# Kernel tuning notes

Measured on AMD Instinct MI355X. Metric: run time of the kernel, lower is better.

Reference implementation:

```python
import jax, jax.numpy as jnp
import numpy as np

N_IMG = 1024
N_VIEWS = 90


def _bilinear(img, yi, xi):
    """Bilinear sample img at float coords (yi=row, xi=col); 0 outside (skimage warp cval=0)."""
    n = img.shape[0]
    y0 = jnp.floor(yi)
    x0 = jnp.floor(xi)
    wy = yi - y0
    wx = xi - x0
    y0i = y0.astype(jnp.int32)
    x0i = x0.astype(jnp.int32)

    def get(yy, xx):
        valid = (yy >= 0) & (yy < n) & (xx >= 0) & (xx < n)
        v = img[jnp.clip(yy, 0, n - 1), jnp.clip(xx, 0, n - 1)]
        return jnp.where(valid, v, jnp.zeros((), img.dtype))

    v00 = get(y0i, x0i)
    v01 = get(y0i, x0i + 1)
    v10 = get(y0i + 1, x0i)
    v11 = get(y0i + 1, x0i + 1)
    return (v00 * (1 - wy) * (1 - wx) + v01 * (1 - wy) * wx
            + v10 * wy * (1 - wx) + v11 * wy * wx)


def radon_jax(image, theta_deg):
    """skimage.transform.radon(image, theta, circle=True) equivalent.
    Rotate image by each angle (bilinear, about center = N//2, inverse map as in
    skimage warp) and sum over rows. Returns sinogram [N, n_angles]."""
    n = image.shape[0]
    center = n // 2
    ang = jnp.deg2rad(theta_deg.astype(image.dtype))
    cos_a = jnp.cos(ang)  # [A]
    sin_a = jnp.sin(ang)
    coords = jnp.arange(n, dtype=image.dtype)
    X, Y = jnp.meshgrid(coords, coords)  # X = col (x), Y = row (y), [N, N]

    def rotate_and_sum(ca, sa):
        # inverse map: src = R @ dst (homogeneous, (x, y) order) as in skimage radon
        x_in = ca * X + sa * Y - center * (ca + sa - 1)
        y_in = -sa * X + ca * Y - center * (ca - sa - 1)
        rotated = _bilinear(image, y_in, x_in)  # [N, N]
        return rotated.sum(axis=0)  # sum over rows -> projection [N]

    sino = jax.vmap(rotate_and_sum)(cos_a, sin_a)  # [A, N]
    return sino.T  # [N, A] to match skimage radon layout


def setup_inputs() -> dict:
    key = jax.random.key(0)
    k1, _ = jax.random.split(key)
    x = jax.random.normal(k1, (N_IMG, N_IMG), dtype=jnp.float32)
    theta = jnp.arange(N_VIEWS, dtype=jnp.float32) * 2.0  # 0..178 deg, 2-deg spacing
    return {"x": x, "theta": theta}


def reference(x, theta):
    return radon_jax(x, theta)
```

## Files before the change

kernel.cpp:

```cpp
#include <hip/hip_runtime.h>

#define N_IMG   1024
#define N_VIEWS 90
#define CENTER  512
#define TILE    64
#define NYB     (N_IMG / TILE)
#define NTHREADS 512
#define NWAVES   8
#define YPT      (TILE / NWAVES)
#define TILE_WORDS 9216

typedef float v2f __attribute__((ext_vector_type(2)));

__device__ __forceinline__ void map_coords(float ca, float sa, float cx, float cy,
                                           float Xf, float Yf,
                                           float& x_in, float& y_in) {
    const float fx0 = fmaf(ca, Xf, cx);
    const float fy0 = fmaf(-sa, Xf, cy);
    x_in = fmaf(sa, Yf, fx0);
    y_in = fmaf(ca, Yf, fy0);
}

__device__ __forceinline__ void gload_lds4(const float* g, float* l) {
    __builtin_amdgcn_global_load_lds((const __attribute__((address_space(1))) void*)g,
                                     (__attribute__((address_space(3))) void*)l, 4, 0, 0);
}
__device__ __forceinline__ void gload_lds16(const float* g, float* l) {
    __builtin_amdgcn_global_load_lds((const __attribute__((address_space(1))) void*)g,
                                     (__attribute__((address_space(3))) void*)l, 16, 0, 0);
}

template<int STRIDE>
__device__ __forceinline__ float sample_tile(const float* __restrict__ tile,
                                             float sa, float ca,
                                             float x_in, float y_in, float basef) {
    const float Sf = (float)STRIDE;
    v2f x2 = {x_in, x_in + sa};
    v2f y2 = {y_in, y_in + ca};
    const v2f dx2 = {2.0f * sa, 2.0f * sa};
    const v2f dy2 = {2.0f * ca, 2.0f * ca};
    const v2f S2  = {Sf, Sf};
    const v2f b2  = {basef, basef};
    v2f acc2 = {0.0f, 0.0f};
    #pragma unroll
    for (int p = 0; p < YPT / 2; ++p) {
        v2f x0f = {floorf(x2.x), floorf(x2.y)};
        v2f y0f = {floorf(y2.x), floorf(y2.y)};
        const v2f wx = x2 - x0f;
        const v2f wy = y2 - y0f;
        const v2f lif = y0f * S2 + x0f + b2;
        const int li0 = (int)lif.x;
        const int li1 = (int)lif.y;
        const v2f t00 = {tile[li0],              tile[li1]};
        const v2f t01 = {tile[li0 + 1],          tile[li1 + 1]};
        const v2f t10 = {tile[li0 + STRIDE],     tile[li1 + STRIDE]};
        const v2f t11 = {tile[li0 + STRIDE + 1], tile[li1 + STRIDE + 1]};
        const v2f top = (t01 - t00) * wx + t00;
        const v2f bot = (t11 - t10) * wx + t10;
        acc2 += (bot - top) * wy + top;
        x2 += dx2; y2 += dy2;
    }
    return acc2.x + acc2.y;
}

__global__ __launch_bounds__(NTHREADS) void radon_tile(const float* __restrict__ img,
                                                       const float* __restrict__ theta,
                                                       float* __restrict__ partial,
                                                       float* __restrict__ out,
                                                       int mode) {
    __shared__ float tile[TILE_WORDS];
    __shared__ float fpar[4];
    __shared__ int   ipar[8];

    const int a  = blockIdx.z;
    const int X0 = blockIdx.x * TILE;
    const int Y0 = blockIdx.y * TILE;
    const int tid  = threadIdx.x;
    const int lane = tid & 63;
    const int wv   = tid >> 6;

    if (wv == 0) {
        const float ang = theta[a] * 0.017453292519943295f;
        float sa, ca;
        __sincosf(ang, &sa, &ca);
        const float cx = (float)CENTER * (1.0f - ca - sa);
        const float cy = (float)CENTER * (1.0f - ca + sa);

        float x00, y00, x01, y01, x10, y10, x11, y11;
        map_coords(ca, sa, cx, cy, (float)X0,        (float)Y0,        x00, y00);
        map_coords(ca, sa, cx, cy, (float)(X0 + 63), (float)Y0,        x01, y01);
        map_coords(ca, sa, cx, cy, (float)X0,        (float)(Y0 + 63), x10, y10);
        map_coords(ca, sa, cx, cy, (float)(X0 + 63), (float)(Y0 + 63), x11, y11);
        const float xmin = fminf(fminf(x00, x01), fminf(x10, x11));
        const float xmax = fmaxf(fmaxf(x00, x01), fmaxf(x10, x11));
        const float ymin = fminf(fminf(y00, y01), fminf(y10, y11));
        const float ymax = fmaxf(fmaxf(y00, y01), fmaxf(y10, y11));

        const int ix0_raw = (int)floorf(xmin);
        const int ix1_raw = (int)floorf(xmax) + 1;
        const int iy0_raw = (int)floorf(ymin);
        const int iy1_raw = (int)floorf(ymax) + 1;

        const bool empty = (ix1_raw < 0) || (ix0_raw > N_IMG - 1) ||
                           (iy1_raw < 0) || (iy0_raw > N_IMG - 1);
        const bool interior = (ix0_raw >= 0) && (ix1_raw <= N_IMG - 1) &&
                              (iy0_raw >= 0) && (iy1_raw <= N_IMG - 1);

        int path = (fabsf(ca) > 0.7072f) ? 0 : ((ca > 0.0f) ? 1 : 2);
        int iy0w, win, dB = 0, ry0 = 0, nrows = 0;
        if (interior) {
            iy0w = iy0_raw;
            if (path == 0) {
                win = min(ix0_raw & ~3, N_IMG - 96);
            } else {
                win = min(ix0_raw, N_IMG - 64);
                dB  = max(win, ix1_raw - 63) - win;
            }
            nrows = iy1_raw - iy0_raw + 1;
        } else {
            iy0w = iy0_raw;
            win  = ix0_raw & ~3;
            ry0  = max(0, iy0_raw);
            nrows = min(N_IMG - 1, iy1_raw) - ry0 + 1;
        }
        if (tid == 0) {
            fpar[0] = sa; fpar[1] = ca; fpar[2] = cx; fpar[3] = cy;
            ipar[0] = iy0w; ipar[1] = nrows; ipar[2] = win; ipar[3] = dB;
            ipar[4] = path;
            ipar[5] = empty ? 1 : (interior ? 2 : 0);
            ipar[6] = ry0;
        }
    }
    __syncthreads();

    float* __restrict__ pslot = partial + ((size_t)(a * NYB + blockIdx.y) << 10) + X0;
    const int flags = ipar[5];

    if (flags & 1) {
        if (mode == 0 && tid < 64) pslot[tid] = 0.0f;
        return;
    }

    const float sa = fpar[0], ca = fpar[1], cx = fpar[2], cy = fpar[3];
    const int iy0 = ipar[0], nrows = ipar[1], win = ipar[2], dB = ipar[3];
    const int path = ipar[4];
    const int S = (path == 0) ? 96 : ((path == 1) ? 95 : 97);

    if (flags & 2) {
        if (path == 0) {
            const int D = nrows * 96;
            for (int o = wv * 256; o < D; o += NWAVES * 256) {
                const int d = o + 4 * lane;
                const int r = (unsigned)d / 96u;
                const int c = d - r * 96;
                const int gr = min(iy0 + r, N_IMG - 1);
                gload_lds16(img + (size_t)gr * N_IMG + win + c, tile + o);
            }
        } else {
            const float* g = img + (size_t)(iy0 + wv) * N_IMG + win + lane;
            float* l = tile + wv * S;
            for (int r = wv; r < nrows; r += NWAVES) {
                gload_lds4(g, l);
                if (dB > 0) gload_lds4(g + dB, l + dB);
                g += NWAVES * N_IMG;
                l += NWAVES * S;
            }
        }
    } else {
        for (int o4 = tid; o4 < TILE_WORDS / 4; o4 += NTHREADS)
            *(float4*)(tile + 4 * o4) = make_float4(0.f, 0.f, 0.f, 0.f);
        __syncthreads();
        const int ry0 = ipar[6];
        const int cx0 = max(0, win);
        const int cxe = min(N_IMG - 1, win + 94);
        const int wIn = cxe - cx0 + 1;
        const int n4  = wIn >> 2;
        const int items = nrows * 24;
        for (int idx = tid; idx < items; idx += NTHREADS) {
            const int r  = (unsigned)idx / 24u;
            const int c4 = idx - r * 24;
            const int gy = ry0 + r;
            float* dst = tile + (gy - iy0) * S + (cx0 - win) + 4 * c4;
            const float* src = img + (size_t)gy * N_IMG + cx0 + 4 * c4;
            if (c4 < n4) {
                *(float4*)dst = *(const float4*)src;
            } else if (c4 == n4) {
                for (int j = 0; j < (wIn & 3); ++j) dst[j] = src[j];
            }
        }
    }
    __syncthreads();

    const float Xf  = (float)(X0 + lane);
    const float fx0 = fmaf(ca, Xf, cx);
    const float fy0 = fmaf(-sa, Xf, cy);
    const float Ybf = (float)(Y0 + wv * YPT);
    const float x_in = fmaf(sa, Ybf, fx0);
    const float y_in = fmaf(ca, Ybf, fy0);
    const float basef = -(float)(iy0 * S + win);

    float acc;
    if (path == 0)      acc = sample_tile<96>(tile, sa, ca, x_in, y_in, basef);
    else if (path == 1) acc = sample_tile<95>(tile, sa, ca, x_in, y_in, basef);
    else                acc = sample_tile<97>(tile, sa, ca, x_in, y_in, basef);

    __syncthreads();
    tile[wv * 64 + lane] = acc;
    __syncthreads();
    if (wv == 0) {
        float s = 0.0f;
        #pragma unroll
        for (int w = 0; w < NWAVES; ++w) s += tile[w * 64 + lane];
        if (mode == 0) pslot[lane] = s;
        else           atomicAdd(&out[(X0 + lane) * N_VIEWS + a], s);
    }
}

__global__ __launch_bounds__(256) void reduce_partials(const float* __restrict__ partial,
                                                       float* __restrict__ out) {
    const int g = blockIdx.x * 256 + threadIdx.x;
    const int a = g >> 10;
    const int X = g & 1023;
    float s = 0.0f;
    #pragma unroll
    for (int yb = 0; yb < NYB; ++yb)
        s += partial[((size_t)(a * NYB + yb) << 10) + X];
    out[X * N_VIEWS + a] = s;
}

extern "C" void kernel_launch(void* const* d_in, const int* in_sizes, int n_in,
                              void* d_out, int out_size, void* d_ws, size_t ws_size,
                              hipStream_t stream) {
    const float* img   = (const float*)d_in[0];
    const float* theta = (const float*)d_in[1];
    float* out     = (float*)d_out;
    float* partial = (float*)d_ws;

    const size_t needed = (size_t)N_VIEWS * NYB * N_IMG * sizeof(float);
    const int mode = (ws_size >= needed) ? 0 : 1;
    if (mode == 1)
        (void)hipMemsetAsync(d_out, 0, (size_t)out_size * sizeof(float), stream);

    dim3 grid(N_IMG / TILE, N_IMG / TILE, N_VIEWS);
    radon_tile<<<grid, NTHREADS, 0, stream>>>(img, theta, partial, out, mode);

    if (mode == 0)
        reduce_partials<<<(N_VIEWS * N_IMG) / 256, 256, 0, stream>>>(partial, out);
}
```

Before: 140.4 us.

## Fuse Y-tile loop into one block per column strip with double-buffered LDS

Each block now handles one angle and one 64-column strip, looping over all 16 Y tiles. While one LDS buffer is sampled, the next tile's image window is prefetched into the other. Per-tile bounds are computed in parallel across lanes and broadcast with shuffles. This removes the partial-sum workspace, the separate reduction kernel and its launch. The cost is a grid of only 1440 blocks, double the LDS per block (which limits occupancy), and serialized per-tile work inside each block.

```diff
diff --git a/kernel.cpp b/kernel.cpp
--- a/kernel.cpp
+++ b/kernel.cpp
@@ -4,7 +4,7 @@
 #define N_VIEWS 90
 #define CENTER  512
 #define TILE    64
-#define NYB     (N_IMG / TILE)
+#define NTX     (N_IMG / TILE)
 #define NTHREADS 512
 #define NWAVES   8
 #define YPT      (TILE / NWAVES)
@@ -63,169 +63,161 @@
     return acc2.x + acc2.y;
 }
 
-__global__ __launch_bounds__(NTHREADS) void radon_tile(const float* __restrict__ img,
-                                                       const float* __restrict__ theta,
-                                                       float* __restrict__ partial,
-                                                       float* __restrict__ out,
-                                                       int mode) {
-    __shared__ float tile[TILE_WORDS];
-    __shared__ float fpar[4];
-    __shared__ int   ipar[8];
-
-    const int a  = blockIdx.z;
-    const int X0 = blockIdx.x * TILE;
-    const int Y0 = blockIdx.y * TILE;
+struct JobP { int win, dB, iy0, nrows, ry0, fl; };
+
+__global__ __launch_bounds__(NTHREADS, 4) void radon_fused(const float* __restrict__ img,
+                                                           const float* __restrict__ theta,
+                                                           float* __restrict__ out) {
+    __shared__ float tile[2][TILE_WORDS];
+
+    const int bx  = blockIdx.x;
+    const int a   = bx >> 4;
+    const int tx  = bx & (NTX - 1);
+    const int X0  = tx * TILE;
     const int tid  = threadIdx.x;
     const int lane = tid & 63;
     const int wv   = tid >> 6;
 
-    if (wv == 0) {
-        const float ang = theta[a] * 0.017453292519943295f;
-        float sa, ca;
-        __sincosf(ang, &sa, &ca);
-        const float cx = (float)CENTER * (1.0f - ca - sa);
-        const float cy = (float)CENTER * (1.0f - ca + sa);
-
-        float x00, y00, x01, y01, x10, y10, x11, y11;
-        map_coords(ca, sa, cx, cy, (float)X0,        (float)Y0,        x00, y00);
-        map_coords(ca, sa, cx, cy, (float)(X0 + 63), (float)Y0,        x01, y01);
-        map_coords(ca, sa, cx, cy, (float)X0,        (float)(Y0 + 63), x10, y10);
-        map_coords(ca, sa, cx, cy, (float)(X0 + 63), (float)(Y0 + 63), x11, y11);
-        const float xmin = fminf(fminf(x00, x01), fminf(x10, x11));
-        const float xmax = fmaxf(fmaxf(x00, x01), fmaxf(x10, x11));
-        const float ymin = fminf(fminf(y00, y01), fminf(y10, y11));
-        const float ymax = fmaxf(fmaxf(y00, y01), fmaxf(y10, y11));
-
-        const int ix0_raw = (int)floorf(xmin);
-        const int ix1_raw = (int)floorf(xmax) + 1;
-        const int iy0_raw = (int)floorf(ymin);
-        const int iy1_raw = (int)floorf(ymax) + 1;
-
-        const bool empty = (ix1_raw < 0) || (ix0_raw > N_IMG - 1) ||
-                           (iy1_raw < 0) || (iy0_raw > N_IMG - 1);
-        const bool interior = (ix0_raw >= 0) && (ix1_raw <= N_IMG - 1) &&
-                              (iy0_raw >= 0) && (iy1_raw <= N_IMG - 1);
-
-        int path = (fabsf(ca) > 0.7072f) ? 0 : ((ca > 0.0f) ? 1 : 2);
-        int iy0w, win, dB = 0, ry0 = 0, nrows = 0;
-        if (interior) {
-            iy0w = iy0_raw;
+    const float ang = theta[a] * 0.017453292519943295f;
+    float sa, ca;
+    __sincosf(ang, &sa, &ca);
+    const float cx = (float)CENTER * (1.0f - ca - sa);
+    const float cy = (float)CENTER * (1.0f - ca + sa);
+    const int path = (fabsf(ca) > 0.7072f) ? 0 : ((ca > 0.0f) ? 1 : 2);
+    const int S = (path == 0) ? 96 : ((path == 1) ? 95 : 97);
+
+    const int tyl = lane & 15;
+    const float Ybase = (float)(tyl * TILE);
+    float x00, y00, x01, y01, x10, y10, x11, y11;
+    map_coords(ca, sa, cx, cy, (float)X0,        Ybase,        x00, y00);
+    map_coords(ca, sa, cx, cy, (float)(X0 + 63), Ybase,        x01, y01);
+    map_coords(ca, sa, cx, cy, (float)X0,        Ybase + 63.f, x10, y10);
+    map_coords(ca, sa, cx, cy, (float)(X0 + 63), Ybase + 63.f, x11, y11);
+    const float xmin = fminf(fminf(x00, x01), fminf(x10, x11));
+    const float xmax = fmaxf(fmaxf(x00, x01), fmaxf(x10, x11));
+    const float ymin = fminf(fminf(y00, y01), fminf(y10, y11));
+    const float ymax = fmaxf(fmaxf(y00, y01), fmaxf(y10, y11));
+
+    const int ix0_raw = (int)floorf(xmin);
+    const int ix1_raw = (int)floorf(xmax) + 1;
+    const int iy0_raw = (int)floorf(ymin);
+    const int iy1_raw = (int)floorf(ymax) + 1;
+
+    const bool empty = (ix1_raw < 0) || (ix0_raw > N_IMG - 1) ||
+                       (iy1_raw < 0) || (iy0_raw > N_IMG - 1);
+    const bool interior = (ix0_raw >= 0) && (ix1_raw <= N_IMG - 1) &&
+                          (iy0_raw >= 0) && (iy1_raw <= N_IMG - 1);
+
+    int winl, dBl = 0, ry0l = 0, nrl = 0, iy0l = iy0_raw;
+    if (interior) {
+        if (path == 0) {
+            winl = min(ix0_raw & ~3, N_IMG - 96);
+        } else {
+            winl = min(ix0_raw, N_IMG - 64);
+            dBl  = max(winl, ix1_raw - 63) - winl;
+        }
+        nrl = iy1_raw - iy0_raw + 1;
+    } else {
+        winl = ix0_raw & ~3;
+        ry0l = max(0, iy0_raw);
+        nrl  = min(N_IMG - 1, iy1_raw) - ry0l + 1;
+    }
+    const int fll = empty ? 1 : (interior ? 2 : 0);
+
+    auto fetch = [&](int ty) -> JobP {
+        JobP p;
+        p.win   = __shfl(winl, ty);
+        p.dB    = __shfl(dBl,  ty);
+        p.iy0   = __shfl(iy0l, ty);
+        p.nrows = __shfl(nrl,  ty);
+        p.ry0   = __shfl(ry0l, ty);
+        p.fl    = __shfl(fll,  ty);
+        return p;
+    };
+
+    auto stage = [&](const JobP& p, float* buf) {
+        if (p.fl & 1) return;
+        if (p.fl & 2) {
             if (path == 0) {
-                win = min(ix0_raw & ~3, N_IMG - 96);
+                const int D = p.nrows * 96;
+                for (int o = wv * 256; o < D; o += NWAVES * 256) {
+                    const int d = o + 4 * lane;
+                    const int r = (unsigned)d / 96u;
+                    const int c = d - r * 96;
+                    const int gr = min(p.iy0 + r, N_IMG - 1);
+                    gload_lds16(img + (size_t)gr * N_IMG + p.win + c, buf + o);
+                }
             } else {
-                win = min(ix0_raw, N_IMG - 64);
-                dB  = max(win, ix1_raw - 63) - win;
-            }
-            nrows = iy1_raw - iy0_raw + 1;
-        } else {
-            iy0w = iy0_raw;
-            win  = ix0_raw & ~3;
-            ry0  = max(0, iy0_raw);
-            nrows = min(N_IMG - 1, iy1_raw) - ry0 + 1;
-        }
-        if (tid == 0) {
-            fpar[0] = sa; fpar[1] = ca; fpar[2] = cx; fpar[3] = cy;
-            ipar[0] = iy0w; ipar[1] = nrows; ipar[2] = win; ipar[3] = dB;
-            ipar[4] = path;
-            ipar[5] = empty ? 1 : (interior ? 2 : 0);
-            ipar[6] = ry0;
-        }
-    }
-    __syncthreads();
-
-    float* __restrict__ pslot = partial + ((size_t)(a * NYB + blockIdx.y) << 10) + X0;
-    const int flags = ipar[5];
-
-    if (flags & 1) {
-        if (mode == 0 && tid < 64) pslot[tid] = 0.0f;
-        return;
-    }
-
-    const float sa = fpar[0], ca = fpar[1], cx = fpar[2], cy = fpar[3];
-    const int iy0 = ipar[0], nrows = ipar[1], win = ipar[2], dB = ipar[3];
-    const int path = ipar[4];
-    const int S = (path == 0) ? 96 : ((path == 1) ? 95 : 97);
-
-    if (flags & 2) {
-        if (path == 0) {
-            const int D = nrows * 96;
-            for (int o = wv * 256; o < D; o += NWAVES * 256) {
-                const int d = o + 4 * lane;
-                const int r = (unsigned)d / 96u;
-                const int c = d - r * 96;
-                const int gr = min(iy0 + r, N_IMG - 1);
-                gload_lds16(img + (size_t)gr * N_IMG + win + c, tile + o);
+                const float* g = img + (size_t)(p.iy0 + wv) * N_IMG + p.win + lane;
+                float* l = buf + wv * S;
+                for (int r = wv; r < p.nrows; r += NWAVES) {
+                    gload_lds4(g, l);
+                    if (p.dB > 0) gload_lds4(g + p.dB, l + p.dB);
+                    g += NWAVES * N_IMG;
+                    l += NWAVES * S;
+                }
             }
         } else {
-            const float* g = img + (size_t)(iy0 + wv) * N_IMG + win + lane;
-            float* l = tile + wv * S;
-            for (int r = wv; r < nrows; r += NWAVES) {
-                gload_lds4(g, l);
-                if (dB > 0) gload_lds4(g + dB, l + dB);
-                g += NWAVES * N_IMG;
-                l += NWAVES * S;
+            for (int o4 = tid; o4 < TILE_WORDS / 4; o4 += NTHREADS)
+                *(float4*)(buf + 4 * o4) = make_float4(0.f, 0.f, 0.f, 0.f);
+            __syncthreads();
+            const int cx0 = max(0, p.win);
+            const int cxe = min(N_IMG - 1, p.win + 94);
+            const int wIn = cxe - cx0 + 1;
+            const int n4  = wIn >> 2;
+            const int items = p.nrows * 24;
+            for (int idx = tid; idx < items; idx += NTHREADS) {
+                const int r  = (unsigned)idx / 24u;
+                const int c4 = idx - r * 24;
+                const int gy = p.ry0 + r;
+                float* dst = buf + (gy - p.iy0) * S + (cx0 - p.win) + 4 * c4;
+                const float* src = img + (size_t)gy * N_IMG + cx0 + 4 * c4;
+                if (c4 < n4) {
+                    *(float4*)dst = *(const float4*)src;
+                } else if (c4 == n4) {
+                    for (int j = 0; j < (wIn & 3); ++j) dst[j] = src[j];
+                }
             }
         }
-    } else {
-        for (int o4 = tid; o4 < TILE_WORDS / 4; o4 += NTHREADS)
-            *(float4*)(tile + 4 * o4) = make_float4(0.f, 0.f, 0.f, 0.f);
-        __syncthreads();
-        const int ry0 = ipar[6];
-        const int cx0 = max(0, win);
-        const int cxe = min(N_IMG - 1, win + 94);
-        const int wIn = cxe - cx0 + 1;
-        const int n4  = wIn >> 2;
-        const int items = nrows * 24;
-        for (int idx = tid; idx < items; idx += NTHREADS) {
-            const int r  = (unsigned)idx / 24u;
-            const int c4 = idx - r * 24;
-            const int gy = ry0 + r;
-            float* dst = tile + (gy - iy0) * S + (cx0 - win) + 4 * c4;
-            const float* src = img + (size_t)gy * N_IMG + cx0 + 4 * c4;
-            if (c4 < n4) {
-                *(float4*)dst = *(const float4*)src;
-            } else if (c4 == n4) {
-                for (int j = 0; j < (wIn & 3); ++j) dst[j] = src[j];
-            }
-        }
-    }
-    __syncthreads();
+    };
 
     const float Xf  = (float)(X0 + lane);
     const float fx0 = fmaf(ca, Xf, cx);
     const float fy0 = fmaf(-sa, Xf, cy);
-    const float Ybf = (float)(Y0 + wv * YPT);
-    const float x_in = fmaf(sa, Ybf, fx0);
-    const float y_in = fmaf(ca, Ybf, fy0);
-    const float basef = -(float)(iy0 * S + win);
-
-    float acc;
-    if (path == 0)      acc = sample_tile<96>(tile, sa, ca, x_in, y_in, basef);
-    else if (path == 1) acc = sample_tile<95>(tile, sa, ca, x_in, y_in, basef);
-    else                acc = sample_tile<97>(tile, sa, ca, x_in, y_in, basef);
-
+    float acc = 0.0f;
+
+    JobP pc = fetch(0);
+    stage(pc, tile[0]);
     __syncthreads();
-    tile[wv * 64 + lane] = acc;
+
+    for (int ty = 0; ty < 16; ++ty) {
+        JobP pn = pc;
+        if (ty < 15) {
+            pn = fetch(ty + 1);
+            stage(pn, tile[(ty + 1) & 1]);
+        }
+        if (!(pc.fl & 1)) {
+            const float Ybf  = (float)(ty * TILE + wv * YPT);
+            const float x_in = fmaf(sa, Ybf, fx0);
+            const float y_in = fmaf(ca, Ybf, fy0);
+            const float basef = -(float)(pc.iy0 * S + pc.win);
+            const float* tl = tile[ty & 1];
+            if (path == 0)      acc += sample_tile<96>(tl, sa, ca, x_in, y_in, basef);
+            else if (path == 1) acc += sample_tile<95>(tl, sa, ca, x_in, y_in, basef);
+            else                acc += sample_tile<97>(tl, sa, ca, x_in, y_in, basef);
+        }
+        __syncthreads();
+        pc = pn;
+    }
+
+    tile[0][wv * 64 + lane] = acc;
     __syncthreads();
     if (wv == 0) {
         float s = 0.0f;
         #pragma unroll
-        for (int w = 0; w < NWAVES; ++w) s += tile[w * 64 + lane];
-        if (mode == 0) pslot[lane] = s;
-        else           atomicAdd(&out[(X0 + lane) * N_VIEWS + a], s);
-    }
-}
-
-__global__ __launch_bounds__(256) void reduce_partials(const float* __restrict__ partial,
-                                                       float* __restrict__ out) {
-    const int g = blockIdx.x * 256 + threadIdx.x;
-    const int a = g >> 10;
-    const int X = g & 1023;
-    float s = 0.0f;
-    #pragma unroll
-    for (int yb = 0; yb < NYB; ++yb)
-        s += partial[((size_t)(a * NYB + yb) << 10) + X];
-    out[X * N_VIEWS + a] = s;
+        for (int w = 0; w < NWAVES; ++w) s += tile[0][w * 64 + lane];
+        out[(X0 + lane) * N_VIEWS + a] = s;
+    }
 }
 
 extern "C" void kernel_launch(void* const* d_in, const int* in_sizes, int n_in,
@@ -233,17 +225,8 @@
                               hipStream_t stream) {
     const float* img   = (const float*)d_in[0];
     const float* theta = (const float*)d_in[1];
-    float* out     = (float*)d_out;
-    float* partial = (float*)d_ws;
-
-    const size_t needed = (size_t)N_VIEWS * NYB * N_IMG * sizeof(float);
-    const int mode = (ws_size >= needed) ? 0 : 1;
-    if (mode == 1)
-        (void)hipMemsetAsync(d_out, 0, (size_t)out_size * sizeof(float), stream);
-
-    dim3 grid(N_IMG / TILE, N_IMG / TILE, N_VIEWS);
-    radon_tile<<<grid, NTHREADS, 0, stream>>>(img, theta, partial, out, mode);
-
-    if (mode == 0)
-        reduce_partials<<<(N_VIEWS * N_IMG) / 256, 256, 0, stream>>>(partial, out);
-}
+    float* out = (float*)d_out;
+    (void)d_ws; (void)ws_size;
+
+    radon_fused<<<dim3(N_VIEWS * NTX), NTHREADS, 0, stream>>>(img, theta, out);
+}
```

Measured after the change: 163.5 us. 16.4% more time.
